# Kernel tuning notes

Hardware: AMD Instinct MI355X
Metric: run time of the kernel (lower is better)

The kernel has to match this reference:

```python
import jax, jax.numpy as jnp
import numpy as np

BN_EPS = 1e-5
LRELU_SLOPE = 0.2
EPS = 1e-8
K = 3


def setup_inputs() -> dict:
    key = jax.random.key(0)
    ks = jax.random.split(key, 8)
    B, Cd, Cs, M, S, N = 8, 256, 512, 4096, 1024, 4096
    return {
        "dense_data": jax.random.normal(ks[0], (B, Cd, M), dtype=jnp.float32),
        "dense_idx": jax.random.randint(ks[1], (B, M), 0, N),
        "sparse_data": jax.random.normal(ks[2], (B, Cs, S), dtype=jnp.float32),
        "sparse_idx": jax.random.randint(ks[3], (B, S), 0, N),
        "pcd": jax.random.normal(ks[4], (B, 3, N), dtype=jnp.float32),
        "conv_w": jax.random.normal(ks[5], (Cd, 3 * Cd), dtype=jnp.float32) * (1.0 / np.sqrt(3 * Cd)),
        "bn_gamma": jnp.ones((Cd,), dtype=jnp.float32),
        "bn_beta": jnp.zeros((Cd,), dtype=jnp.float32),
    }


def _knn_interpolate(dense_xyz, sparse_xyz, sparse_feats, k):
    # dense_xyz: [B,3,M], sparse_xyz: [B,3,S], sparse_feats: [B,Cs,S]
    d2 = (
        jnp.sum(dense_xyz**2, axis=1)[:, :, None]
        + jnp.sum(sparse_xyz**2, axis=1)[:, None, :]
        - 2.0 * jnp.einsum("bdm,bds->bms", dense_xyz, sparse_xyz)
    )  # [B,M,S] squared distances
    neg_d, idx = jax.lax.top_k(-d2, k)  # [B,M,K]
    d_nb = -neg_d
    w = 1.0 / (d_nb + EPS)
    w = w / jnp.sum(w, axis=-1, keepdims=True)  # [B,M,K]
    # gather neighbor features: [B,Cs,M,K]
    nb = jnp.take_along_axis(sparse_feats[:, :, None, :], idx[:, None, :, :], axis=3)
    return jnp.sum(nb * w[:, None, :, :], axis=-1)  # [B,Cs,M]


def reference(dense_data, dense_idx, sparse_data, sparse_idx, pcd, conv_w, bn_gamma, bn_beta):
    # gather xyz coords of dense / sparse points: [B,3,M], [B,3,S]
    dense_xyz = jnp.take_along_axis(pcd, dense_idx[:, None, :], axis=2)
    sparse_xyz = jnp.take_along_axis(pcd, sparse_idx[:, None, :], axis=2)
    interp = _knn_interpolate(dense_xyz, sparse_xyz, sparse_data, K)  # [B,Cs,M]
    x = jnp.concatenate([dense_data, interp], axis=1)  # [B,3*Cd,M]
    # 1x1 conv (no bias)
    y = jnp.einsum("oc,bcm->bom", conv_w, x)
    # BatchNorm1d (training mode: batch statistics over B and M, biased var)
    mu = jnp.mean(y, axis=(0, 2), keepdims=True)
    var = jnp.mean((y - mu) ** 2, axis=(0, 2), keepdims=True)
    y = (y - mu) * jax.lax.rsqrt(var + BN_EPS)
    y = y * bn_gamma[None, :, None] + bn_beta[None, :, None]
    # LeakyReLU(0.2)
    y = jnp.where(y >= 0, y, LRELU_SLOPE * y)
    return (y, dense_idx)
```

## Files before the change

kernel.cpp:

```cpp
#include <hip/hip_runtime.h>
#include <float.h>

#define DEVI __device__ __forceinline__

namespace {

constexpr int NB   = 8;
constexpr int CD   = 256;
constexpr int CS   = 512;
constexpr int MM   = 4096;
constexpr int SS   = 1024;
constexpr int NN   = 4096;
constexpr int KTOT = 768;
constexpr int OC   = 256;
constexpr float KEPS  = 1e-8f;
constexpr float BNEPS = 1e-5f;
constexpr float SLOPE = 0.2f;

constexpr size_t OFF_Z    = 0;
constexpr size_t SZ_Z     = (size_t)NB * SS * OC * 4;
constexpr size_t OFF_IDX3 = OFF_Z + SZ_Z;
constexpr size_t SZ_IDX3  = (size_t)NB * MM * 3 * 4;
constexpr size_t OFF_W3   = OFF_IDX3 + SZ_IDX3;
constexpr size_t OFF_WBF  = OFF_W3 + SZ_IDX3;
constexpr size_t SZ_WBF   = (size_t)OC * KTOT * 2;
constexpr size_t OFF_PS   = OFF_WBF + SZ_WBF;
constexpr size_t SZ_PS    = (size_t)512 * OC * 4;
constexpr size_t OFF_PS2  = OFF_PS + SZ_PS;
constexpr size_t OFF_MU   = OFF_PS2 + SZ_PS;
constexpr size_t OFF_RS   = OFF_MU + 1024;

typedef __attribute__((ext_vector_type(8))) short s16x8;
typedef __attribute__((ext_vector_type(4))) float f32x4;

DEVI short f2bf(float f) {
  union { float f; unsigned u; } c; c.f = f;
  unsigned r = c.u + 0x7fffu + ((c.u >> 16) & 1u);
  return (short)(r >> 16);
}

__global__ void k_wcast(const float* __restrict__ w, short* __restrict__ wbf) {
  int i = blockIdx.x * 256 + threadIdx.x;
  wbf[i] = f2bf(w[i]);
}

__global__ __launch_bounds__(256) void k_knn(
    const int* __restrict__ didx, const int* __restrict__ sidx,
    const float* __restrict__ pcd,
    int* __restrict__ idx3, float* __restrict__ w3,
    float* __restrict__ outIdxF) {
  __shared__ float4 sxyz[SS];
  __shared__ float  pd[4][64][3];
  __shared__ int    pi[4][64][3];

  int blk = blockIdx.x;
  int b   = blk >> 6;
  int m0  = (blk & 63) << 6;
  int tid = threadIdx.x;
  const float* pb = pcd + (size_t)b * 3 * NN;

  for (int s = tid; s < SS; s += 256) {
    int si = sidx[b * SS + s];
    sxyz[s] = make_float4(pb[si], pb[NN + si], pb[2 * NN + si], 0.f);
  }

  int p     = tid & 63;
  int chunk = tid >> 6;
  int m     = m0 + p;
  int di    = didx[b * MM + m];
  float px = pb[di], py = pb[NN + di], pz = pb[2 * NN + di];

  if (chunk == 0) outIdxF[b * MM + m] = (float)di;

  __syncthreads();

  float d0 = FLT_MAX, d1 = FLT_MAX, d2 = FLT_MAX;
  int   i0 = 0, i1 = 0, i2 = 0;
  int s0c = chunk << 8;
#pragma unroll 4
  for (int t = 0; t < 256; ++t) {
    int s = s0c + t;
    float4 c = sxyz[s];
    float dx = c.x - px, dy = c.y - py, dz = c.z - pz;
    float d  = dx * dx + dy * dy + dz * dz;
    bool lt0 = d < d0, lt1 = d < d1, lt2 = d < d2;
    d2 = lt1 ? d1 : (lt2 ? d : d2);  i2 = lt1 ? i1 : (lt2 ? s : i2);
    d1 = lt0 ? d0 : (lt1 ? d : d1);  i1 = lt0 ? i0 : (lt1 ? s : i1);
    d0 = lt0 ? d  : d0;              i0 = lt0 ? s : i0;
  }
  pd[chunk][p][0] = d0; pd[chunk][p][1] = d1; pd[chunk][p][2] = d2;
  pi[chunk][p][0] = i0; pi[chunk][p][1] = i1; pi[chunk][p][2] = i2;
  __syncthreads();

  if (tid < 64) {
    float e0 = FLT_MAX, e1 = FLT_MAX, e2 = FLT_MAX;
    int   j0 = 0, j1 = 0, j2 = 0;
#pragma unroll
    for (int c = 0; c < 4; ++c)
#pragma unroll
      for (int r = 0; r < 3; ++r) {
        float d = pd[c][p][r]; int s = pi[c][p][r];
        bool lt0 = d < e0, lt1 = d < e1, lt2 = d < e2;
        e2 = lt1 ? e1 : (lt2 ? d : e2);  j2 = lt1 ? j1 : (lt2 ? s : j2);
        e1 = lt0 ? e0 : (lt1 ? d : e1);  j1 = lt0 ? j0 : (lt1 ? s : j1);
        e0 = lt0 ? d  : e0;              j0 = lt0 ? s : j0;
      }
    float w0 = 1.f / (e0 + KEPS), w1 = 1.f / (e1 + KEPS), w2 = 1.f / (e2 + KEPS);
    float inv = 1.f / (w0 + w1 + w2);
    int base = (b * MM + m) * 3;
    idx3[base] = j0; idx3[base + 1] = j1; idx3[base + 2] = j2;
    w3[base] = w0 * inv; w3[base + 1] = w1 * inv; w3[base + 2] = w2 * inv;
  }
}

__global__ __launch_bounds__(256) void k_gemmZ(
    const float* __restrict__ sp, const short* __restrict__ wbf,
    float* __restrict__ Z) {
  __shared__ __align__(16) short Wl[256 * 72];
  __shared__ __align__(16) short Sl[32 * 72];

  int blk = blockIdx.x;
  int st = blk & 31, b = blk >> 5;
  int s0 = st * 32;
  int tid = threadIdx.x, wv = tid >> 6, lane = tid & 63;
  int lo = lane & 15, quad = lane >> 4;

  f32x4 acc[4][2] = {};
  for (int k0 = 0; k0 < CS; k0 += 64) {
    __syncthreads();
#pragma unroll
    for (int r = 0; r < 8; ++r) {
      int lin = r * 256 + tid, row = lin >> 3, c8 = lin & 7;
      uint4 v = *(const uint4*)((const unsigned short*)wbf + (size_t)row * KTOT + CD + k0 + c8 * 8);
      *(uint4*)(&Wl[row * 72 + c8 * 8]) = v;
    }
#pragma unroll
    for (int r = 0; r < 2; ++r) {
      int lin = r * 256 + tid, cc = lin >> 3, s4 = lin & 7;
      float4 v = *(const float4*)(sp + (size_t)(b * CS + k0 + cc) * SS + s0 + s4 * 4);
      Sl[(s4 * 4 + 0) * 72 + cc] = f2bf(v.x);
      Sl[(s4 * 4 + 1) * 72 + cc] = f2bf(v.y);
      Sl[(s4 * 4 + 2) * 72 + cc] = f2bf(v.z);
      Sl[(s4 * 4 + 3) * 72 + cc] = f2bf(v.w);
    }
    __syncthreads();
    s16x8 af[2][4], bfr[2][2];
#pragma unroll
    for (int h = 0; h < 2; ++h) {
#pragma unroll
      for (int i = 0; i < 4; ++i)
        af[h][i] = *(const s16x8*)(&Wl[(wv * 64 + i * 16 + lo) * 72 + h * 32 + quad * 8]);
#pragma unroll
      for (int j = 0; j < 2; ++j)
        bfr[h][j] = *(const s16x8*)(&Sl[(j * 16 + lo) * 72 + h * 32 + quad * 8]);
    }
#pragma unroll
    for (int h = 0; h < 2; ++h)
#pragma unroll
      for (int i = 0; i < 4; ++i)
#pragma unroll
        for (int j = 0; j < 2; ++j)
          acc[i][j] = __builtin_amdgcn_mfma_f32_16x16x32_bf16(af[h][i], bfr[h][j], acc[i][j], 0, 0, 0);
  }
#pragma unroll
  for (int i = 0; i < 4; ++i)
#pragma unroll
    for (int j = 0; j < 2; ++j) {
      int s = j * 16 + lo, o = wv * 64 + i * 16 + quad * 4;
      *(f32x4*)(Z + (size_t)(b * SS + s0 + s) * OC + o) = acc[i][j];
    }
}

__global__ __launch_bounds__(256) void k_gemmDC(
    const float* __restrict__ dense, const float* __restrict__ Z,
    const int* __restrict__ idx3, const float* __restrict__ w3,
    const short* __restrict__ wbf, float* __restrict__ y,
    float* __restrict__ ps, float* __restrict__ ps2) {
  __shared__ __align__(16) short Wl[256 * 72];
  __shared__ __align__(16) short Xl[64 * 72];
  __shared__ int   mi3[192];
  __shared__ float mw3[192];

  int blk = blockIdx.x;
  int mt = blk & 63, b = blk >> 6, m0 = mt << 6;
  int tid = threadIdx.x, wv = tid >> 6, lane = tid & 63;
  int lo = lane & 15, quad = lane >> 4;

  {
    int base = (b * MM + m0) * 3;
    for (int i = tid; i < 192; i += 256) { mi3[i] = idx3[base + i]; mw3[i] = w3[base + i]; }
  }

  f32x4 acc[4][4] = {};
  for (int k0 = 0; k0 < CD; k0 += 64) {
    __syncthreads();
#pragma unroll
    for (int r = 0; r < 8; ++r) {
      int lin = r * 256 + tid, row = lin >> 3, c8 = lin & 7;
      uint4 v = *(const uint4*)((const unsigned short*)wbf + (size_t)row * KTOT + k0 + c8 * 8);
      *(uint4*)(&Wl[row * 72 + c8 * 8]) = v;
    }
#pragma unroll
    for (int r = 0; r < 4; ++r) {
      int lin = r * 256 + tid, kk = lin >> 4, m4 = lin & 15;
      float4 v = *(const float4*)(dense + (size_t)(b * CD + k0 + kk) * MM + m0 + m4 * 4);
      Xl[(m4 * 4 + 0) * 72 + kk] = f2bf(v.x);
      Xl[(m4 * 4 + 1) * 72 + kk] = f2bf(v.y);
      Xl[(m4 * 4 + 2) * 72 + kk] = f2bf(v.z);
      Xl[(m4 * 4 + 3) * 72 + kk] = f2bf(v.w);
    }
    __syncthreads();
    s16x8 af[2][4], bfr[2][4];
#pragma unroll
    for (int h = 0; h < 2; ++h) {
#pragma unroll
      for (int i = 0; i < 4; ++i)
        af[h][i] = *(const s16x8*)(&Wl[(wv * 64 + i * 16 + lo) * 72 + h * 32 + quad * 8]);
#pragma unroll
      for (int j = 0; j < 4; ++j)
        bfr[h][j] = *(const s16x8*)(&Xl[(j * 16 + lo) * 72 + h * 32 + quad * 8]);
    }
#pragma unroll
    for (int h = 0; h < 2; ++h)
#pragma unroll
      for (int i = 0; i < 4; ++i)
#pragma unroll
        for (int j = 0; j < 4; ++j)
          acc[i][j] = __builtin_amdgcn_mfma_f32_16x16x32_bf16(af[h][i], bfr[h][j], acc[i][j], 0, 0, 0);
  }

  float* P = (float*)Wl;
  const float* Zb = Z + (size_t)b * SS * OC;
  float ss[4][4] = {}, s2s[4][4] = {};
  __syncthreads();

#pragma unroll
  for (int h = 0; h < 2; ++h) {
#pragma unroll 4
    for (int ml = 0; ml < 32; ++ml) {
      int mg = (h * 32 + ml) * 3;
      float p = mw3[mg + 0] * Zb[(size_t)mi3[mg + 0] * OC + tid]
              + mw3[mg + 1] * Zb[(size_t)mi3[mg + 1] * OC + tid]
              + mw3[mg + 2] * Zb[(size_t)mi3[mg + 2] * OC + tid];
      P[ml * 260 + tid] = p;
    }
    __syncthreads();
#pragma unroll
    for (int i = 0; i < 4; ++i)
#pragma unroll
      for (int jj = 0; jj < 2; ++jj) {
        int j = h * 2 + jj, ml = jj * 16 + lo;
        int o = wv * 64 + i * 16 + quad * 4;
        f32x4 p = *(const f32x4*)(&P[ml * 260 + o]);
        f32x4 v = acc[i][j] + p;
        float* dst = y + ((size_t)(b * OC + o)) * MM + m0 + j * 16 + lo;
#pragma unroll
        for (int r = 0; r < 4; ++r) {
          float vv = v[r];
          dst[(size_t)r * MM] = vv;
          ss[i][r] += vv; s2s[i][r] += vv * vv;
        }
      }
    __syncthreads();
  }

#pragma unroll
  for (int i = 0; i < 4; ++i)
#pragma unroll
    for (int r = 0; r < 4; ++r) {
      float a = ss[i][r], q = s2s[i][r];
      for (int off = 1; off < 16; off <<= 1) { a += __shfl_xor(a, off); q += __shfl_xor(q, off); }
      ss[i][r] = a; s2s[i][r] = q;
    }
  if (lo == 0) {
#pragma unroll
    for (int i = 0; i < 4; ++i)
#pragma unroll
      for (int r = 0; r < 4; ++r) {
        int o = wv * 64 + i * 16 + quad * 4 + r;
        ps[blk * OC + o]  = ss[i][r];
        ps2[blk * OC + o] = s2s[i][r];
      }
  }
}

__global__ void k_finalize(const float* __restrict__ ps, const float* __restrict__ ps2,
                           float* __restrict__ mu, float* __restrict__ rs) {
  int o = threadIdx.x;
  float s = 0.f, s2 = 0.f;
#pragma unroll 8
  for (int k = 0; k < 512; ++k) { s += ps[k * OC + o]; s2 += ps2[k * OC + o]; }
  float mn = s / (float)(NB * MM);
  float vr = s2 / (float)(NB * MM) - mn * mn;
  mu[o] = mn;
  rs[o] = rsqrtf(vr + BNEPS);
}

__global__ void k_norm(float* __restrict__ y, const float* __restrict__ mu,
                       const float* __restrict__ rs, const float* __restrict__ gamma,
                       const float* __restrict__ beta) {
  int i = blockIdx.x * 256 + threadIdx.x;
  int o = (i >> 10) & 255;
  float mn = mu[o], a = rs[o] * gamma[o], be = beta[o];
  float4 v = ((const float4*)y)[i];
  float t;
  t = (v.x - mn) * a + be; v.x = t >= 0.f ? t : SLOPE * t;
  t = (v.y - mn) * a + be; v.y = t >= 0.f ? t : SLOPE * t;
  t = (v.z - mn) * a + be; v.z = t >= 0.f ? t : SLOPE * t;
  t = (v.w - mn) * a + be; v.w = t >= 0.f ? t : SLOPE * t;
  ((float4*)y)[i] = v;
}

}

extern "C" void kernel_launch(void* const* d_in, const int* in_sizes, int n_in,
                              void* d_out, int out_size, void* d_ws, size_t ws_size,
                              hipStream_t stream) {
  const float* dense = (const float*)d_in[0];
  const int*   didx  = (const int*)d_in[1];
  const float* sp    = (const float*)d_in[2];
  const int*   sidx  = (const int*)d_in[3];
  const float* pcd   = (const float*)d_in[4];
  const float* convw = (const float*)d_in[5];
  const float* gamma = (const float*)d_in[6];
  const float* beta  = (const float*)d_in[7];

  float* y = (float*)d_out;
  float* outIdxF = y + (size_t)NB * OC * MM;

  char* ws = (char*)d_ws;
  float* Z    = (float*)(ws + OFF_Z);
  int*   idx3 = (int*)(ws + OFF_IDX3);
  float* w3   = (float*)(ws + OFF_W3);
  short* wbf  = (short*)(ws + OFF_WBF);
  float* ps   = (float*)(ws + OFF_PS);
  float* ps2  = (float*)(ws + OFF_PS2);
  float* mu   = (float*)(ws + OFF_MU);
  float* rs   = (float*)(ws + OFF_RS);

  k_wcast   <<<(OC * KTOT) / 256, 256, 0, stream>>>(convw, wbf);
  k_knn     <<<NB * (MM / 64), 256, 0, stream>>>(didx, sidx, pcd, idx3, w3, outIdxF);
  k_gemmZ   <<<NB * (SS / 32), 256, 0, stream>>>(sp, wbf, Z);
  k_gemmDC  <<<NB * (MM / 64), 256, 0, stream>>>(dense, Z, idx3, w3, wbf, y, ps, ps2);
  k_finalize<<<1, 256, 0, stream>>>(ps, ps2, mu, rs);
  k_norm    <<<(NB * OC * MM / 4) / 256, 256, 0, stream>>>(y, mu, rs, gamma, beta);
}
```

Measured before the change: 192.1 us.

## Fuse GEMM, BatchNorm statistics and normalization into one cooperative kernel

The weight bf16 cast moves into the kNN kernel, and the dense GEMM, BN statistics reduction and normalize+LeakyReLU are merged into one cooperative kernel that keeps accumulators in registers across two grid-wide syncs. The separate finalize and norm kernels go away, along with the extra full read and write of the output tensor. This trades those passes for grid-sync overhead and the need for all 512 blocks to be co-resident, which may fail or limit occupancy because the kernel holds a large accumulator set.

```diff
diff --git a/kernel.cpp b/kernel.cpp
--- a/kernel.cpp
+++ b/kernel.cpp
@@ -1,7 +1,10 @@
 #include <hip/hip_runtime.h>
+#include <hip/hip_cooperative_groups.h>
 #include <float.h>
 
 #define DEVI __device__ __forceinline__
+
+namespace cg = cooperative_groups;
 
 namespace {
 
@@ -27,8 +30,8 @@
 constexpr size_t OFF_PS   = OFF_WBF + SZ_WBF;
 constexpr size_t SZ_PS    = (size_t)512 * OC * 4;
 constexpr size_t OFF_PS2  = OFF_PS + SZ_PS;
-constexpr size_t OFF_MU   = OFF_PS2 + SZ_PS;
-constexpr size_t OFF_RS   = OFF_MU + 1024;
+constexpr size_t OFF_A    = OFF_PS2 + SZ_PS;
+constexpr size_t OFF_B    = OFF_A + 1024;
 
 typedef __attribute__((ext_vector_type(8))) short s16x8;
 typedef __attribute__((ext_vector_type(4))) float f32x4;
@@ -39,16 +42,12 @@
   return (short)(r >> 16);
 }
 
-__global__ void k_wcast(const float* __restrict__ w, short* __restrict__ wbf) {
-  int i = blockIdx.x * 256 + threadIdx.x;
-  wbf[i] = f2bf(w[i]);
-}
-
 __global__ __launch_bounds__(256) void k_knn(
     const int* __restrict__ didx, const int* __restrict__ sidx,
     const float* __restrict__ pcd,
     int* __restrict__ idx3, float* __restrict__ w3,
-    float* __restrict__ outIdxF) {
+    float* __restrict__ outIdxF,
+    const float* __restrict__ convw, short* __restrict__ wbf) {
   __shared__ float4 sxyz[SS];
   __shared__ float  pd[4][64][3];
   __shared__ int    pi[4][64][3];
@@ -58,6 +57,11 @@
   int m0  = (blk & 63) << 6;
   int tid = threadIdx.x;
   const float* pb = pcd + (size_t)b * 3 * NN;
+
+  for (int i = tid; i < 384; i += 256) {
+    int g = blk * 384 + i;
+    wbf[g] = f2bf(convw[g]);
+  }
 
   for (int s = tid; s < SS; s += 256) {
     int si = sidx[b * SS + s];
@@ -171,15 +175,19 @@
     }
 }
 
-__global__ __launch_bounds__(256) void k_gemmDC(
+__global__ __launch_bounds__(256) void k_coop(
     const float* __restrict__ dense, const float* __restrict__ Z,
     const int* __restrict__ idx3, const float* __restrict__ w3,
     const short* __restrict__ wbf, float* __restrict__ y,
-    float* __restrict__ ps, float* __restrict__ ps2) {
+    float* __restrict__ ps, float* __restrict__ ps2,
+    float* __restrict__ sA, float* __restrict__ sB,
+    const float* __restrict__ gamma, const float* __restrict__ beta) {
   __shared__ __align__(16) short Wl[256 * 72];
   __shared__ __align__(16) short Xl[64 * 72];
   __shared__ int   mi3[192];
   __shared__ float mw3[192];
+
+  cg::grid_group grid = cg::this_grid();
 
   int blk = blockIdx.x;
   int mt = blk & 63, b = blk >> 6, m0 = mt << 6;
@@ -231,7 +239,6 @@
 
   float* P = (float*)Wl;
   const float* Zb = Z + (size_t)b * SS * OC;
-  float ss[4][4] = {}, s2s[4][4] = {};
   __syncthreads();
 
 #pragma unroll
@@ -251,64 +258,87 @@
       for (int jj = 0; jj < 2; ++jj) {
         int j = h * 2 + jj, ml = jj * 16 + lo;
         int o = wv * 64 + i * 16 + quad * 4;
-        f32x4 p = *(const f32x4*)(&P[ml * 260 + o]);
-        f32x4 v = acc[i][j] + p;
-        float* dst = y + ((size_t)(b * OC + o)) * MM + m0 + j * 16 + lo;
+        acc[i][j] += *(const f32x4*)(&P[ml * 260 + o]);
+      }
+    __syncthreads();
+  }
+
+  {
+    float ss[4][4] = {}, s2s[4][4] = {};
+#pragma unroll
+    for (int i = 0; i < 4; ++i)
+#pragma unroll
+      for (int j = 0; j < 4; ++j)
 #pragma unroll
         for (int r = 0; r < 4; ++r) {
-          float vv = v[r];
-          dst[(size_t)r * MM] = vv;
-          ss[i][r] += vv; s2s[i][r] += vv * vv;
+          float v = acc[i][j][r];
+          ss[i][r] += v; s2s[i][r] += v * v;
         }
+#pragma unroll
+    for (int i = 0; i < 4; ++i)
+#pragma unroll
+      for (int r = 0; r < 4; ++r) {
+        float a = ss[i][r], q = s2s[i][r];
+        for (int off = 1; off < 16; off <<= 1) { a += __shfl_xor(a, off); q += __shfl_xor(q, off); }
+        ss[i][r] = a; s2s[i][r] = q;
       }
-    __syncthreads();
-  }
-
-#pragma unroll
-  for (int i = 0; i < 4; ++i)
-#pragma unroll
-    for (int r = 0; r < 4; ++r) {
-      float a = ss[i][r], q = s2s[i][r];
-      for (int off = 1; off < 16; off <<= 1) { a += __shfl_xor(a, off); q += __shfl_xor(q, off); }
-      ss[i][r] = a; s2s[i][r] = q;
-    }
-  if (lo == 0) {
-#pragma unroll
-    for (int i = 0; i < 4; ++i)
+    if (lo == 0) {
+#pragma unroll
+      for (int i = 0; i < 4; ++i)
+#pragma unroll
+        for (int r = 0; r < 4; ++r) {
+          int o = wv * 64 + i * 16 + quad * 4 + r;
+          ps[(size_t)blk * OC + o]  = ss[i][r];
+          ps2[(size_t)blk * OC + o] = s2s[i][r];
+        }
+    }
+  }
+
+  grid.sync();
+
+  if (blk < 8) {
+    float* red = (float*)Xl;
+    int oo = (blk << 5) + (tid & 31), sl = tid >> 5;
+    float a = 0.f, q = 0.f;
+#pragma unroll 4
+    for (int j = 0; j < 64; ++j) {
+      int k = sl * 64 + j;
+      a += ps[(size_t)k * OC + oo];
+      q += ps2[(size_t)k * OC + oo];
+    }
+    red[sl * 32 + (tid & 31)] = a;
+    red[256 + sl * 32 + (tid & 31)] = q;
+    __syncthreads();
+    if (tid < 32) {
+      float S = 0.f, S2 = 0.f;
+#pragma unroll
+      for (int s = 0; s < 8; ++s) { S += red[s * 32 + tid]; S2 += red[256 + s * 32 + tid]; }
+      int o = (blk << 5) + tid;
+      float mn = S / (float)(NB * MM);
+      float vr = S2 / (float)(NB * MM) - mn * mn;
+      float aa = rsqrtf(vr + BNEPS) * gamma[o];
+      sA[o] = aa;
+      sB[o] = beta[o] - mn * aa;
+    }
+  }
+
+  grid.sync();
+
+#pragma unroll
+  for (int i = 0; i < 4; ++i) {
+    int o = wv * 64 + i * 16 + quad * 4;
+    f32x4 A  = *(const f32x4*)(sA + o);
+    f32x4 Bv = *(const f32x4*)(sB + o);
+#pragma unroll
+    for (int j = 0; j < 4; ++j) {
+      float* dst = y + (size_t)(b * OC + o) * MM + m0 + j * 16 + lo;
 #pragma unroll
       for (int r = 0; r < 4; ++r) {
-        int o = wv * 64 + i * 16 + quad * 4 + r;
-        ps[blk * OC + o]  = ss[i][r];
-        ps2[blk * OC + o] = s2s[i][r];
+        float t = acc[i][j][r] * A[r] + Bv[r];
+        dst[(size_t)r * MM] = t >= 0.f ? t : SLOPE * t;
       }
-  }
-}
-
-__global__ void k_finalize(const float* __restrict__ ps, const float* __restrict__ ps2,
-                           float* __restrict__ mu, float* __restrict__ rs) {
-  int o = threadIdx.x;
-  float s = 0.f, s2 = 0.f;
-#pragma unroll 8
-  for (int k = 0; k < 512; ++k) { s += ps[k * OC + o]; s2 += ps2[k * OC + o]; }
-  float mn = s / (float)(NB * MM);
-  float vr = s2 / (float)(NB * MM) - mn * mn;
-  mu[o] = mn;
-  rs[o] = rsqrtf(vr + BNEPS);
-}
-
-__global__ void k_norm(float* __restrict__ y, const float* __restrict__ mu,
-                       const float* __restrict__ rs, const float* __restrict__ gamma,
-                       const float* __restrict__ beta) {
-  int i = blockIdx.x * 256 + threadIdx.x;
-  int o = (i >> 10) & 255;
-  float mn = mu[o], a = rs[o] * gamma[o], be = beta[o];
-  float4 v = ((const float4*)y)[i];
-  float t;
-  t = (v.x - mn) * a + be; v.x = t >= 0.f ? t : SLOPE * t;
-  t = (v.y - mn) * a + be; v.y = t >= 0.f ? t : SLOPE * t;
-  t = (v.z - mn) * a + be; v.z = t >= 0.f ? t : SLOPE * t;
-  t = (v.w - mn) * a + be; v.w = t >= 0.f ? t : SLOPE * t;
-  ((float4*)y)[i] = v;
+    }
+  }
 }
 
 }
@@ -335,13 +365,15 @@
   short* wbf  = (short*)(ws + OFF_WBF);
   float* ps   = (float*)(ws + OFF_PS);
   float* ps2  = (float*)(ws + OFF_PS2);
-  float* mu   = (float*)(ws + OFF_MU);
-  float* rs   = (float*)(ws + OFF_RS);
-
-  k_wcast   <<<(OC * KTOT) / 256, 256, 0, stream>>>(convw, wbf);
-  k_knn     <<<NB * (MM / 64), 256, 0, stream>>>(didx, sidx, pcd, idx3, w3, outIdxF);
-  k_gemmZ   <<<NB * (SS / 32), 256, 0, stream>>>(sp, wbf, Z);
-  k_gemmDC  <<<NB * (MM / 64), 256, 0, stream>>>(dense, Z, idx3, w3, wbf, y, ps, ps2);
-  k_finalize<<<1, 256, 0, stream>>>(ps, ps2, mu, rs);
-  k_norm    <<<(NB * OC * MM / 4) / 256, 256, 0, stream>>>(y, mu, rs, gamma, beta);
-}
+  float* sA   = (float*)(ws + OFF_A);
+  float* sB   = (float*)(ws + OFF_B);
+
+  k_knn  <<<NB * (MM / 64), 256, 0, stream>>>(didx, sidx, pcd, idx3, w3, outIdxF, convw, wbf);
+  k_gemmZ<<<NB * (SS / 32), 256, 0, stream>>>(sp, wbf, Z);
+
+  void* args[] = {(void*)&dense, (void*)&Z, (void*)&idx3, (void*)&w3, (void*)&wbf,
+                  (void*)&y, (void*)&ps, (void*)&ps2, (void*)&sA, (void*)&sB,
+                  (void*)&gamma, (void*)&beta};
+  hipLaunchCooperativeKernel((const void*)k_coop, dim3(NB * (MM / 64)), dim3(256),
+                             args, 0, stream);
+}
```

After: 277.5 us. 44.5% more time.
